# Optimization experiments

Measured on AMD Instinct MI355X. Metric: run time of the kernel, lower is better.

The kernel has to match this reference:

```python
import jax, jax.numpy as jnp
import numpy as np

TAU = 2.0          # LIF membrane time constant (decay_input=True)
VTH = 1.0          # spiking threshold (hidden layers); last layer has inf threshold
EPS = 1e-5         # batchnorm eps
ALPHA = 2.0        # ATan surrogate-gradient alpha
HL = 8             # HLfreq_ratio (chunk length in timesteps)
SIZES = [1024, 1024, 512]

@jax.custom_vjp
def spike(x):
    return (x >= 0).astype(x.dtype)

def _spike_fwd(x):
    return (x >= 0).astype(x.dtype), x

def _spike_bwd(x, g):
    # spikingjelly ATan surrogate: alpha/2 / (1 + (pi/2 * alpha * x)^2)
    return (g * (ALPHA / 2.0) / (1.0 + (jnp.pi / 2.0 * ALPHA * x) ** 2),)

spike.defvjp(_spike_fwd, _spike_bwd)

def setup_inputs() -> dict:
    key = jax.random.key(0)
    ks = jax.random.split(key, 1 + len(SIZES))
    T, B, D = 1024, 32, 512
    inp = {"x": jax.random.normal(ks[0], (T, B, D), dtype=jnp.float32)}
    d_in = D
    for i, s in enumerate(SIZES):
        inp[f"W{i}"] = jax.random.normal(ks[i + 1], (s, d_in), dtype=jnp.float32) / np.float32(np.sqrt(d_in))
        inp[f"b{i}"] = jnp.zeros((s,), jnp.float32)
        inp[f"g{i}"] = jnp.ones((s,), jnp.float32)    # BN gamma
        inp[f"bt{i}"] = jnp.zeros((s,), jnp.float32)  # BN beta
        d_in = s
    return inp

def _forward(x, params):
    # x: [T, B, d_in]; process chunks of HL timesteps, membrane state carried across chunks
    n_chunks = x.shape[0] // HL
    B = x.shape[1]
    xr = x.reshape(n_chunks, HL, B, x.shape[2])
    n_layers = len(params)
    vs0 = tuple(jnp.zeros((B, p[0].shape[0]), x.dtype) for p in params)

    def chunk_step(vs, xc):  # xc: [HL, B, d_in]
        h = xc
        new_vs = []
        for i, (W, b, g, bt) in enumerate(params):
            # Linear over all timesteps of the chunk
            h = jnp.einsum('tbd,ed->tbe', h, W) + b
            # BatchNorm (training mode): stats over (time, batch) of this chunk, per channel
            mu = h.mean((0, 1))
            var = jnp.mean((h - mu) ** 2, (0, 1))
            h = g * (h - mu) * jax.lax.rsqrt(var + EPS) + bt
            last = (i == n_layers - 1)

            def step(v, xt, last=last):
                v = v + (xt - v) / TAU          # decay_input=True LIF charge
                if last:
                    return v, v                 # inf threshold: pure leaky integrator, emit v_seq
                s = spike(v - VTH)
                return v * (1.0 - s), s         # hard reset to v_reset=0

            v_new, h = jax.lax.scan(step, vs[i], h)
            new_vs.append(v_new)
        # reduction_mode='mean_mempot': mean of last layer's v_seq over chunk timesteps
        return tuple(new_vs), h.mean(0)

    _, z = jax.lax.scan(chunk_step, vs0, xr)
    return z  # [n_chunks, B, d_output]

def reference(x, W0, b0, g0, bt0, W1, b1, g1, bt1, W2, b2, g2, bt2):
    params = [(W0, b0, g0, bt0), (W1, b1, g1, bt1), (W2, b2, g2, bt2)]
    return _forward(x, params)
```

## Files before the change

### kernel.cpp

```cpp
#include <hip/hip_runtime.h>
#include <hip/hip_bf16.h>
#include <stdint.h>


__global__ void k_zero(unsigned int* __restrict__ p, int n){
  int i = blockIdx.x * 256 + threadIdx.x;
  if (i < n) p[i] = 0u;
}

__global__ void k_transpose(const float* __restrict__ in, float* __restrict__ out, int R, int C){
  __shared__ float tile[32][33];
  int bx = blockIdx.x * 32, by = blockIdx.y * 32;
  int tx = threadIdx.x, ty = threadIdx.y;
  for (int i = ty; i < 32; i += 8)
    tile[i][tx] = in[(size_t)(by + i) * C + bx + tx];
  __syncthreads();
  for (int i = ty; i < 32; i += 8)
    out[(size_t)(bx + i) * R + by + tx] = tile[tx][i];
}

__global__ __launch_bounds__(256) void k_gemm_np(const float* __restrict__ A,
    const float* __restrict__ Bw, const float* __restrict__ bias,
    float* __restrict__ C, int M){
  (void)M;
  __shared__ float As[32][129];
  __shared__ float Bs[32][65];
  int bm = blockIdx.y * 128;
  int bn = blockIdx.x * 64;
  int tid = threadIdx.x;
  int kk = tid & 31, g = tid >> 5;
  int tm = tid >> 4, tn = tid & 15;
  float acc[8][4];
#pragma unroll
  for (int ii = 0; ii < 8; ++ii)
#pragma unroll
    for (int jj = 0; jj < 4; ++jj) acc[ii][jj] = 0.f;

  for (int k0 = 0; k0 < 512; k0 += 32){
#pragma unroll
    for (int rr = 0; rr < 16; ++rr)
      As[kk][g + rr * 8] = A[(size_t)(bm + g + rr * 8) * 512 + k0 + kk];
#pragma unroll
    for (int rr = 0; rr < 8; ++rr)
      Bs[kk][g + rr * 8] = Bw[(size_t)(bn + g + rr * 8) * 512 + k0 + kk];
    __syncthreads();
#pragma unroll
    for (int k = 0; k < 32; ++k){
      float a[8], b[4];
#pragma unroll
      for (int ii = 0; ii < 8; ++ii) a[ii] = As[k][tm * 8 + ii];
#pragma unroll
      for (int jj = 0; jj < 4; ++jj) b[jj] = Bs[k][tn * 4 + jj];
#pragma unroll
      for (int ii = 0; ii < 8; ++ii)
#pragma unroll
        for (int jj = 0; jj < 4; ++jj)
          acc[ii][jj] = __fmaf_rn(a[ii], b[jj], acc[ii][jj]);
    }
    __syncthreads();
  }
#pragma unroll
  for (int ii = 0; ii < 8; ++ii){
    size_t m = (size_t)(bm + tm * 8 + ii);
#pragma unroll
    for (int jj = 0; jj < 4; ++jj){
      int e = bn + tn * 4 + jj;
      C[m * 1024 + e] = __fadd_rn(acc[ii][jj], bias[e]);
    }
  }
}

__global__ __launch_bounds__(256) void k_stats_np(const float* __restrict__ A,
    float* __restrict__ mu, float* __restrict__ var, int Dch, int c0){
  int cl = blockIdx.x;
  int ch = blockIdx.y * 256 + threadIdx.x;
  const float* base = A + (size_t)cl * 256 * Dch + ch;
  float acc = 0.f;
  for (int s = 0; s < 256; ++s)
    acc = __fadd_rn(acc, base[(size_t)s * Dch]);
  float m = __fmul_rn(acc, 1.f / 256.f);
  float vacc = 0.f;
  for (int s = 0; s < 256; ++s){
    float d = __fsub_rn(base[(size_t)s * Dch], m);
    vacc = __fadd_rn(vacc, __fmul_rn(d, d));
  }
  int c = c0 + cl;
  mu[(size_t)c * Dch + ch]  = m;
  var[(size_t)c * Dch + ch] = __fmul_rn(vacc, 1.f / 256.f);
}

__global__ __launch_bounds__(64) void k_scan_spike_np(const float* __restrict__ A,
    const float* __restrict__ mu, const float* __restrict__ var,
    const float* __restrict__ g, const float* __restrict__ bt,
    float* __restrict__ vstate, unsigned long long* __restrict__ mask,
    int Dch, int c0, int nb){
  int ebn = Dch >> 6;
  int eb = blockIdx.x % ebn;
  int b  = blockIdx.x / ebn;
  int e  = (eb << 6) + threadIdx.x;
  float gg = g[e], bb = bt[e];
  float v = vstate[(size_t)b * Dch + e];
  float hbuf[8];
#pragma unroll
  for (int t = 0; t < 8; ++t)
    hbuf[t] = A[(size_t)(t * 32 + b) * Dch + e];
  for (int cl = 0; cl < nb; ++cl){
    int c = c0 + cl;
    float m  = mu[(size_t)c * Dch + e];
    float ve = __fadd_rn(var[(size_t)c * Dch + e], 1e-5f);
    float sq = (float)sqrt((double)ve);
    float r  = (float)(1.0 / (double)sq);
    float hn[8];
    if (cl + 1 < nb){
#pragma unroll
      for (int t = 0; t < 8; ++t)
        hn[t] = A[(size_t)(((cl + 1) * 8 + t) * 32 + b) * Dch + e];
    } else {
#pragma unroll
      for (int t = 0; t < 8; ++t) hn[t] = 0.f;
    }
#pragma unroll
    for (int t = 0; t < 8; ++t){
      int sl = (cl * 8 + t) * 32 + b;
      float xn = __fadd_rn(__fmul_rn(__fmul_rn(gg, __fsub_rn(hbuf[t], m)), r), bb);
      v = __fadd_rn(v, __fmul_rn(__fsub_rn(xn, v), 0.5f));
      bool sp = (v >= 1.0f);
      unsigned long long bal = __ballot(sp);
      if (sp) v = 0.0f;
      if (threadIdx.x == 0) mask[(size_t)sl * 16 + eb] = bal;
    }
#pragma unroll
    for (int t = 0; t < 8; ++t) hbuf[t] = hn[t];
  }
  vstate[(size_t)b * Dch + e] = v;
}

__global__ __launch_bounds__(256) void k_sparse_np(const unsigned long long* __restrict__ mask,
    const float* __restrict__ WT, const float* __restrict__ bias,
    float* __restrict__ C, int Dout){
  int tid = threadIdx.x;
  int lane = tid & 63;
  int wid = tid >> 6;
  int wps = Dout >> 8;
  int chgrp = wid % wps;
  int sgrp  = wid / wps;
  int spb   = 4 / wps;
  int s = blockIdx.x * spb + sgrp;
  int ch = (chgrp << 8) + (lane << 2);
  __shared__ unsigned short list[2][1024];
  __shared__ int nlist[2];

  if (lane == 0 && chgrp == 0){
    const unsigned long long* mrow = mask + (size_t)s * 16;
    int n = 0;
    for (int w = 0; w < 16; ++w){
      unsigned long long msk = mrow[w];
      while (msk){
        int bit = __ffsll((unsigned long long)msk) - 1;
        msk &= msk - 1;
        list[sgrp][n++] = (unsigned short)(w * 64 + bit);
      }
    }
    nlist[sgrp] = n;
  }
  __syncthreads();
  int n = nlist[sgrp];
  const unsigned short* il = list[sgrp];
  float a0 = 0.f, a1 = 0.f, a2 = 0.f, a3 = 0.f;
  int i = 0;
  for (; i + 4 <= n; i += 4){
    int d0 = il[i], d1 = il[i + 1], d2 = il[i + 2], d3 = il[i + 3];
    float4 w0 = *(const float4*)(WT + (size_t)d0 * Dout + ch);
    float4 w1 = *(const float4*)(WT + (size_t)d1 * Dout + ch);
    float4 w2 = *(const float4*)(WT + (size_t)d2 * Dout + ch);
    float4 w3 = *(const float4*)(WT + (size_t)d3 * Dout + ch);
    a0 = __fadd_rn(a0, w0.x); a1 = __fadd_rn(a1, w0.y); a2 = __fadd_rn(a2, w0.z); a3 = __fadd_rn(a3, w0.w);
    a0 = __fadd_rn(a0, w1.x); a1 = __fadd_rn(a1, w1.y); a2 = __fadd_rn(a2, w1.z); a3 = __fadd_rn(a3, w1.w);
    a0 = __fadd_rn(a0, w2.x); a1 = __fadd_rn(a1, w2.y); a2 = __fadd_rn(a2, w2.z); a3 = __fadd_rn(a3, w2.w);
    a0 = __fadd_rn(a0, w3.x); a1 = __fadd_rn(a1, w3.y); a2 = __fadd_rn(a2, w3.z); a3 = __fadd_rn(a3, w3.w);
  }
  for (; i < n; ++i){
    int d = il[i];
    float4 wv = *(const float4*)(WT + (size_t)d * Dout + ch);
    a0 = __fadd_rn(a0, wv.x); a1 = __fadd_rn(a1, wv.y); a2 = __fadd_rn(a2, wv.z); a3 = __fadd_rn(a3, wv.w);
  }
  float4 bb = *(const float4*)(bias + ch);
  float4 o;
  o.x = __fadd_rn(a0, bb.x);
  o.y = __fadd_rn(a1, bb.y);
  o.z = __fadd_rn(a2, bb.z);
  o.w = __fadd_rn(a3, bb.w);
  *(float4*)(C + (size_t)s * Dout + ch) = o;
}

__global__ __launch_bounds__(64) void k_scan_last_np(const float* __restrict__ A,
    const float* __restrict__ mu, const float* __restrict__ var,
    const float* __restrict__ g, const float* __restrict__ bt,
    float* __restrict__ vstate, float* __restrict__ out, int c0, int nb){
  const int Dch = 512;
  int eb = blockIdx.x & 7;
  int b  = blockIdx.x >> 3;
  int e  = (eb << 6) + threadIdx.x;
  float gg = g[e], bb = bt[e];
  float v = vstate[(size_t)b * Dch + e];
  float hbuf[8];
#pragma unroll
  for (int t = 0; t < 8; ++t)
    hbuf[t] = A[(size_t)(t * 32 + b) * Dch + e];
  for (int cl = 0; cl < nb; ++cl){
    int c = c0 + cl;
    float m  = mu[(size_t)c * Dch + e];
    float ve = __fadd_rn(var[(size_t)c * Dch + e], 1e-5f);
    float sq = (float)sqrt((double)ve);
    float r  = (float)(1.0 / (double)sq);
    float hn[8];
    if (cl + 1 < nb){
#pragma unroll
      for (int t = 0; t < 8; ++t)
        hn[t] = A[(size_t)(((cl + 1) * 8 + t) * 32 + b) * Dch + e];
    } else {
#pragma unroll
      for (int t = 0; t < 8; ++t) hn[t] = 0.f;
    }
    float macc = 0.f;
#pragma unroll
    for (int t = 0; t < 8; ++t){
      float xn = __fadd_rn(__fmul_rn(__fmul_rn(gg, __fsub_rn(hbuf[t], m)), r), bb);
      v = __fadd_rn(v, __fmul_rn(__fsub_rn(xn, v), 0.5f));
      macc = __fadd_rn(macc, v);
    }
    out[((size_t)c * 32 + b) * 512 + e] = __fmul_rn(macc, 0.125f);
#pragma unroll
    for (int t = 0; t < 8; ++t) hbuf[t] = hn[t];
  }
  vstate[(size_t)b * Dch + e] = v;
}

static inline size_t al256(size_t x){ return (x + 255) & ~(size_t)255; }

extern "C" void kernel_launch(void* const* d_in, const int* in_sizes, int n_in,
                              void* d_out, int out_size, void* d_ws, size_t ws_size,
                              hipStream_t stream){
  (void)in_sizes; (void)n_in; (void)out_size;
  const float* x   = (const float*)d_in[0];
  const float* W0  = (const float*)d_in[1];
  const float* b0  = (const float*)d_in[2];
  const float* g0  = (const float*)d_in[3];
  const float* bt0 = (const float*)d_in[4];
  const float* W1  = (const float*)d_in[5];
  const float* b1  = (const float*)d_in[6];
  const float* g1  = (const float*)d_in[7];
  const float* bt1 = (const float*)d_in[8];
  const float* W2  = (const float*)d_in[9];
  const float* b2  = (const float*)d_in[10];
  const float* g2  = (const float*)d_in[11];
  const float* bt2 = (const float*)d_in[12];
  float* out = (float*)d_out;

  char* p = (char*)d_ws;
  auto carve = [&](size_t bytes)->char*{ char* q = p; p += al256(bytes); return q; };
  float* W1T  = (float*)carve((size_t)1024 * 1024 * 4);
  float* W2T  = (float*)carve((size_t)1024 * 512 * 4);
  float* mu0  = (float*)carve((size_t)128 * 1024 * 4);
  float* var0 = (float*)carve((size_t)128 * 1024 * 4);
  float* mu1  = (float*)carve((size_t)128 * 1024 * 4);
  float* var1 = (float*)carve((size_t)128 * 1024 * 4);
  float* mu2  = (float*)carve((size_t)128 * 512 * 4);
  float* var2 = (float*)carve((size_t)128 * 512 * 4);
  float* v0   = (float*)carve((size_t)32 * 1024 * 4);
  float* v1   = (float*)carve((size_t)32 * 1024 * 4);
  float* v2   = (float*)carve((size_t)32 * 512 * 4);
  size_t fixed_used = (size_t)(p - (char*)d_ws);

  auto need = [&](int nb)->size_t{
    return al256((size_t)nb * 256 * 1024 * 4)
         + 2 * al256((size_t)nb * 256 * 16 * 8);
  };
  int NB = 128;
  while (NB > 1 && fixed_used + need(NB) > ws_size) NB >>= 1;
  if (fixed_used + need(NB) > ws_size) return;

  float*              a_buf = (float*)carve((size_t)NB * 256 * 1024 * 4);
  unsigned long long* mask0 = (unsigned long long*)carve((size_t)NB * 256 * 16 * 8);
  unsigned long long* mask1 = (unsigned long long*)carve((size_t)NB * 256 * 16 * 8);

  {
    int nz = 32 * (1024 + 1024 + 512);
    k_zero<<<dim3((nz + 255) / 256), dim3(256), 0, stream>>>((unsigned int*)v0, nz);
  }
  k_transpose<<<dim3(32, 32), dim3(32, 8), 0, stream>>>(W1, W1T, 1024, 1024);
  k_transpose<<<dim3(32, 16), dim3(32, 8), 0, stream>>>(W2, W2T, 512, 1024);

  int nblk = 128 / NB;
  for (int cb = 0; cb < nblk; ++cb){
    int c0 = cb * NB;
    int M = NB * 256;
    const float* xblk = x + (size_t)c0 * 256 * 512;

    k_gemm_np<<<dim3(16, M / 128), dim3(256), 0, stream>>>(xblk, W0, b0, a_buf, M);
    k_stats_np<<<dim3(NB, 4), dim3(256), 0, stream>>>(a_buf, mu0, var0, 1024, c0);
    k_scan_spike_np<<<dim3(32 * 16), dim3(64), 0, stream>>>(a_buf, mu0, var0, g0, bt0, v0, mask0, 1024, c0, NB);

    k_sparse_np<<<dim3(M), dim3(256), 0, stream>>>(mask0, W1T, b1, a_buf, 1024);
    k_stats_np<<<dim3(NB, 4), dim3(256), 0, stream>>>(a_buf, mu1, var1, 1024, c0);
    k_scan_spike_np<<<dim3(32 * 16), dim3(64), 0, stream>>>(a_buf, mu1, var1, g1, bt1, v1, mask1, 1024, c0, NB);

    k_sparse_np<<<dim3(M / 2), dim3(256), 0, stream>>>(mask1, W2T, b2, a_buf, 512);
    k_stats_np<<<dim3(NB, 2), dim3(256), 0, stream>>>(a_buf, mu2, var2, 512, c0);
    k_scan_last_np<<<dim3(32 * 8), dim3(64), 0, stream>>>(a_buf, mu2, var2, g2, bt2, v2, out, c0, NB);
  }
}
```

Measured before the change: 1.297 ms.

## Replace layer-0 shared-memory GEMM with register-tiled GEMM over transposed inputs

```diff
diff --git a/kernel.cpp b/kernel.cpp
--- a/kernel.cpp
+++ b/kernel.cpp
@@ -19,53 +19,81 @@
     out[(size_t)(bx + i) * R + by + tx] = tile[tx][i];
 }
 
-__global__ __launch_bounds__(256) void k_gemm_np(const float* __restrict__ A,
-    const float* __restrict__ Bw, const float* __restrict__ bias,
+__device__ __forceinline__ void fma16x4(const float4& a, const float* b, float acc[4][16]){
+#pragma unroll
+  for (int j = 0; j < 4; ++j){
+    const float av = j == 0 ? a.x : (j == 1 ? a.y : (j == 2 ? a.z : a.w));
+#pragma unroll
+    for (int i = 0; i < 16; ++i)
+      acc[j][i] = __fmaf_rn(av, b[i], acc[j][i]);
+  }
+}
+
+__global__ __launch_bounds__(256, 4) void k_gemm_sm(const float* __restrict__ xT,
+    const float* __restrict__ W0T, const float* __restrict__ bias,
     float* __restrict__ C, int M){
-  (void)M;
-  __shared__ float As[32][129];
-  __shared__ float Bs[32][65];
-  int bm = blockIdx.y * 128;
-  int bn = blockIdx.x * 64;
-  int tid = threadIdx.x;
-  int kk = tid & 31, g = tid >> 5;
-  int tm = tid >> 4, tn = tid & 15;
-  float acc[8][4];
-#pragma unroll
-  for (int ii = 0; ii < 8; ++ii)
-#pragma unroll
-    for (int jj = 0; jj < 4; ++jj) acc[ii][jj] = 0.f;
-
-  for (int k0 = 0; k0 < 512; k0 += 32){
-#pragma unroll
-    for (int rr = 0; rr < 16; ++rr)
-      As[kk][g + rr * 8] = A[(size_t)(bm + g + rr * 8) * 512 + k0 + kk];
-#pragma unroll
-    for (int rr = 0; rr < 8; ++rr)
-      Bs[kk][g + rr * 8] = Bw[(size_t)(bn + g + rr * 8) * 512 + k0 + kk];
+  __shared__ float S[128 * 68];
+  const int tid  = threadIdx.x;
+  const int lane = tid & 63;
+  const int w    = tid >> 6;
+  const int bn   = blockIdx.x * 64;
+  const int bm   = blockIdx.y * 256;
+  int e0 = __builtin_amdgcn_readfirstlane(bn + w * 16);
+  const float* __restrict__ Arow = xT + bm + lane * 4;
+  const float* __restrict__ Wrow = W0T + e0;
+
+  float acc[4][16];
+#pragma unroll
+  for (int j = 0; j < 4; ++j)
+#pragma unroll
+    for (int i = 0; i < 16; ++i) acc[j][i] = 0.f;
+
+  float4 aA = *(const float4*)(Arow);
+  float bA[16], bB[16];
+#pragma unroll
+  for (int i = 0; i < 16; ++i) bA[i] = Wrow[i];
+
+  for (int k = 0; k < 512; k += 2){
+    float4 aB = *(const float4*)(Arow + (size_t)(k + 1) * M);
+#pragma unroll
+    for (int i = 0; i < 16; ++i) bB[i] = Wrow[(k + 1) * 1024 + i];
+    fma16x4(aA, bA, acc);
+    if (k + 2 < 512){
+      aA = *(const float4*)(Arow + (size_t)(k + 2) * M);
+#pragma unroll
+      for (int i = 0; i < 16; ++i) bA[i] = Wrow[(k + 2) * 1024 + i];
+    }
+    fma16x4(aB, bB, acc);
+  }
+
+#pragma unroll
+  for (int i = 0; i < 16; ++i){
+    const float bi = bias[e0 + i];
+#pragma unroll
+    for (int j = 0; j < 4; ++j) acc[j][i] = __fadd_rn(acc[j][i], bi);
+  }
+
+#pragma unroll
+  for (int t = 0; t < 2; ++t){
+    if (t) __syncthreads();
+    if ((lane >> 5) == t){
+      const int lm4 = (lane & 31) * 4;
+#pragma unroll
+      for (int j = 0; j < 4; ++j)
+#pragma unroll
+        for (int i4 = 0; i4 < 4; ++i4)
+          *(float4*)&S[(lm4 + j) * 68 + (w * 16 + i4 * 4)] =
+            make_float4(acc[j][i4 * 4 + 0], acc[j][i4 * 4 + 1],
+                        acc[j][i4 * 4 + 2], acc[j][i4 * 4 + 3]);
+    }
     __syncthreads();
 #pragma unroll
-    for (int k = 0; k < 32; ++k){
-      float a[8], b[4];
-#pragma unroll
-      for (int ii = 0; ii < 8; ++ii) a[ii] = As[k][tm * 8 + ii];
-#pragma unroll
-      for (int jj = 0; jj < 4; ++jj) b[jj] = Bs[k][tn * 4 + jj];
-#pragma unroll
-      for (int ii = 0; ii < 8; ++ii)
-#pragma unroll
-        for (int jj = 0; jj < 4; ++jj)
-          acc[ii][jj] = __fmaf_rn(a[ii], b[jj], acc[ii][jj]);
-    }
-    __syncthreads();
-  }
-#pragma unroll
-  for (int ii = 0; ii < 8; ++ii){
-    size_t m = (size_t)(bm + tm * 8 + ii);
-#pragma unroll
-    for (int jj = 0; jj < 4; ++jj){
-      int e = bn + tn * 4 + jj;
-      C[m * 1024 + e] = __fadd_rn(acc[ii][jj], bias[e]);
+    for (int u = 0; u < 8; ++u){
+      int idx = u * 256 + tid;
+      int row = idx >> 4;
+      int c4  = (idx & 15) << 2;
+      float4 v = *(const float4*)&S[row * 68 + c4];
+      *(float4*)&C[(size_t)(bm + t * 128 + row) * 1024 + (bn + c4)] = v;
     }
   }
 }
@@ -259,6 +287,7 @@
 
   char* p = (char*)d_ws;
   auto carve = [&](size_t bytes)->char*{ char* q = p; p += al256(bytes); return q; };
+  float* W0T  = (float*)carve((size_t)512 * 1024 * 4);
   float* W1T  = (float*)carve((size_t)1024 * 1024 * 4);
   float* W2T  = (float*)carve((size_t)1024 * 512 * 4);
   float* mu0  = (float*)carve((size_t)128 * 1024 * 4);
@@ -274,6 +303,7 @@
 
   auto need = [&](int nb)->size_t{
     return al256((size_t)nb * 256 * 1024 * 4)
+         + al256((size_t)nb * 256 * 512 * 4)
          + 2 * al256((size_t)nb * 256 * 16 * 8);
   };
   int NB = 128;
@@ -281,6 +311,7 @@
   if (fixed_used + need(NB) > ws_size) return;
 
   float*              a_buf = (float*)carve((size_t)NB * 256 * 1024 * 4);
+  float*              xT    = (float*)carve((size_t)NB * 256 * 512 * 4);
   unsigned long long* mask0 = (unsigned long long*)carve((size_t)NB * 256 * 16 * 8);
   unsigned long long* mask1 = (unsigned long long*)carve((size_t)NB * 256 * 16 * 8);
 
@@ -288,6 +319,7 @@
     int nz = 32 * (1024 + 1024 + 512);
     k_zero<<<dim3((nz + 255) / 256), dim3(256), 0, stream>>>((unsigned int*)v0, nz);
   }
+  k_transpose<<<dim3(16, 32), dim3(32, 8), 0, stream>>>(W0, W0T, 1024, 512);
   k_transpose<<<dim3(32, 32), dim3(32, 8), 0, stream>>>(W1, W1T, 1024, 1024);
   k_transpose<<<dim3(32, 16), dim3(32, 8), 0, stream>>>(W2, W2T, 512, 1024);
 
@@ -297,7 +329,8 @@
     int M = NB * 256;
     const float* xblk = x + (size_t)c0 * 256 * 512;
 
-    k_gemm_np<<<dim3(16, M / 128), dim3(256), 0, stream>>>(xblk, W0, b0, a_buf, M);
+    k_transpose<<<dim3(16, M / 32), dim3(32, 8), 0, stream>>>(xblk, xT, M, 512);
+    k_gemm_sm<<<dim3(16, M / 256), dim3(256), 0, stream>>>(xT, W0T, b0, a_buf, M);
     k_stats_np<<<dim3(NB, 4), dim3(256), 0, stream>>>(a_buf, mu0, var0, 1024, c0);
     k_scan_spike_np<<<dim3(32 * 16), dim3(64), 0, stream>>>(a_buf, mu0, var0, g0, bt0, v0, mask0, 1024, c0, NB);
 
```

Measured after the change: 1.221 ms. -5.9%, faster.
